# Kernel optimization log

Measured on AMD Instinct MI355X. Metric: run time of the kernel, lower is better.

Reference implementation:

```python
import jax, jax.numpy as jnp
import numpy as np

B, S, H = 1, 2048, 1024
NH, NKV, D = 8, 2, 128           # query heads, kv heads, head_dim
E, TOPK = 64, 6                   # experts per modality, top-k
IT, IV, IS = 512, 256, 1024       # text / vision expert inter, shared inter (=512*2)
THETA = 500000.0
SECTIONS = (22, 22, 20)           # h, w, t rotary freq split; sum = D//2
EPS = 1e-5


def rmsnorm(x, w):
    return x * w * jax.lax.rsqrt(jnp.mean(x * x, axis=-1, keepdims=True) + EPS)


def apply_mrope(x, positions):
    # x: [B,S,h,D]; positions: [3,B,S] (h, w, t position streams)
    inv_freq = 1.0 / (THETA ** (jnp.arange(0, D, 2, dtype=jnp.float32) / D))  # [D//2]
    axis_idx = np.repeat(np.arange(3), SECTIONS)              # which pos stream per freq band
    pos = jnp.transpose(positions[axis_idx], (1, 2, 0)).astype(jnp.float32)  # [B,S,D//2]
    freqs = pos * inv_freq
    cos = jnp.cos(freqs)[:, :, None, :]
    sin = jnp.sin(freqs)[:, :, None, :]
    x1, x2 = x[..., 0::2], x[..., 1::2]                       # interleaved (non-neox)
    o1 = x1 * cos - x2 * sin
    o2 = x1 * sin + x2 * cos
    return jnp.stack([o1, o2], axis=-1).reshape(x.shape)


def attention(x, positions, w_qkv, w_o):
    b, s, _ = x.shape
    qkv = x @ w_qkv
    q, k, v = jnp.split(qkv, [NH * D, NH * D + NKV * D], axis=-1)
    q = q.reshape(b, s, NH, D)
    k = k.reshape(b, s, NKV, D)
    v = v.reshape(b, s, NKV, D)
    q = apply_mrope(q, positions)
    k = apply_mrope(k, positions)
    rep = NH // NKV
    k = jnp.repeat(k, rep, axis=2)
    v = jnp.repeat(v, rep, axis=2)
    scores = jnp.einsum('bqhd,bkhd->bhqk', q, k) * (D ** -0.5)
    causal = jnp.tril(jnp.ones((s, s), bool))
    scores = jnp.where(causal, scores, -jnp.inf)
    attn = jax.nn.softmax(scores, axis=-1)
    out = jnp.einsum('bhqk,bkhd->bqhd', attn, v).reshape(b, s, NH * D)
    return out @ w_o


def mlp(x, wg, wu, wd):
    return (jax.nn.silu(x @ wg) * (x @ wu)) @ wd


def moe_branch(x, gate_w, bias, wg, wu, wd):
    # x: [T,H]; gate_w: [H,E] fp32; bias: [E] fp32 correction bias
    logits = x.astype(jnp.float32) @ gate_w                   # [T,E]
    scores = jax.nn.sigmoid(logits)
    _, topi = jax.lax.top_k(scores + bias[None, :], TOPK)     # bias only picks experts
    w = jnp.take_along_axis(scores, topi, axis=-1)            # weights from raw scores
    w = w / jnp.sum(w, axis=-1, keepdims=True)                # renormalize
    T = x.shape[0]
    gates = jnp.zeros((T, E), jnp.float32).at[jnp.arange(T)[:, None], topi].set(w)
    g = jax.nn.silu(jnp.einsum('th,ehi->eti', x, wg)) * jnp.einsum('th,ehi->eti', x, wu)
    g = g * gates.T[:, :, None].astype(x.dtype)               # fold routing weights pre-down-proj
    return jnp.einsum('eti,eih->th', g, wd)


def _forward(hidden_states, positions, visual_token_mask, w_qkv, w_o, ln1_w, ln2_w,
             text_gate_w, vision_gate_w, corr_bias, tw_gate, tw_up, tw_down,
             vw_gate, vw_up, vw_down, sw_gate, sw_up, sw_down):
    h = hidden_states + attention(rmsnorm(hidden_states, ln1_w), positions, w_qkv, w_o)
    x = rmsnorm(h, ln2_w).reshape(-1, H)                      # [T,H]
    shared = mlp(x, sw_gate, sw_up, sw_down)
    text_out = moe_branch(x, text_gate_w, corr_bias[0], tw_gate, tw_up, tw_down)
    vision_out = moe_branch(x, vision_gate_w, corr_bias[1], vw_gate, vw_up, vw_down)
    mask = visual_token_mask.reshape(-1, 1)
    moe_out = jnp.where(mask, vision_out, text_out) + shared
    return h + moe_out.reshape(h.shape)


def setup_inputs() -> dict:
    key = jax.random.key(0)
    ks = jax.random.split(key, 16)
    rn = lambda i, shape, s: jax.random.normal(ks[i], shape, jnp.float32) * s
    return dict(
        hidden_states=rn(0, (B, S, H), 1.0),
        positions=jnp.broadcast_to(jnp.arange(S, dtype=jnp.int32)[None, None, :], (3, B, S)),
        visual_token_mask=jax.random.bernoulli(ks[1], 0.3, (B, S)),
        w_qkv=rn(2, (H, (NH + 2 * NKV) * D), H ** -0.5),
        w_o=rn(3, (NH * D, H), (NH * D) ** -0.5),
        ln1_w=jnp.ones((H,), jnp.float32),
        ln2_w=jnp.ones((H,), jnp.float32),
        text_gate_w=rn(4, (H, E), H ** -0.5),
        vision_gate_w=rn(5, (H, E), H ** -0.5),
        corr_bias=rn(6, (2, E), 0.02),
        tw_gate=rn(7, (E, H, IT), H ** -0.5),
        tw_up=rn(8, (E, H, IT), H ** -0.5),
        tw_down=rn(9, (E, IT, H), IT ** -0.5),
        vw_gate=rn(10, (E, H, IV), H ** -0.5),
        vw_up=rn(11, (E, H, IV), H ** -0.5),
        vw_down=rn(12, (E, IV, H), IV ** -0.5),
        sw_gate=rn(13, (H, IS), H ** -0.5),
        sw_up=rn(14, (H, IS), H ** -0.5),
        sw_down=rn(15, (IS, H), IS ** -0.5),
    )


def reference(hidden_states, positions, visual_token_mask, w_qkv, w_o, ln1_w, ln2_w,
              text_gate_w, vision_gate_w, corr_bias, tw_gate, tw_up, tw_down,
              vw_gate, vw_up, vw_down, sw_gate, sw_up, sw_down):
    return _forward(hidden_states, positions, visual_token_mask, w_qkv, w_o, ln1_w, ln2_w,
                    text_gate_w, vision_gate_w, corr_bias, tw_gate, tw_up, tw_down,
                    vw_gate, vw_up, vw_down, sw_gate, sw_up, sw_down)
```

## Files before the change

### kernel.cpp

```cpp
#include <hip/hip_runtime.h>
#include <hip/hip_bf16.h>
#include <math.h>

#define TT   2048
#define HID  1024
#define NHEAD 8
#define NKVH  2
#define HD   128
#define QKVN 1536
#define NEXP 64
#define NTOP 6
#define I_T  512
#define I_V  256
#define I_S  1024
#define SBASE ((size_t)12288 * 512)
#define NCHUNK 576

typedef unsigned short u16;
typedef __attribute__((ext_vector_type(8))) short short8v;
typedef __attribute__((ext_vector_type(4))) float f32x4;

__device__ inline u16 f2bf(float f) {
  __hip_bfloat16 h = __float2bfloat16(f);
  return *reinterpret_cast<u16*>(&h);
}
__device__ inline float bfu2f(u16 u) {
  unsigned x = ((unsigned)u) << 16;
  return __uint_as_float(x);
}
__device__ inline void split2(float f, u16& h, u16& l) {
  h = f2bf(f);
  l = f2bf(f - bfu2f(h));
}
__device__ inline void split8(const float* f, u16* h, u16* l) {
#pragma unroll
  for (int i = 0; i < 8; ++i) split2(f[i], h[i], l[i]);
}

__device__ inline f32x4 mfma16(short8v a, short8v b, f32x4 c) {
  return __builtin_amdgcn_mfma_f32_16x16x32_bf16(a, b, c, 0, 0, 0);
}

__device__ inline void wload64(const float* __restrict__ W, int ldw, int c0, int kc,
                               float4* r) {
  const int t = threadIdx.x;
  const int c4 = (t & 15) << 2;
  const int r0 = t >> 4;
#pragma unroll
  for (int j = 0; j < 8; ++j)
    r[j] = *(const float4*)&W[(size_t)(kc + r0 + j * 16) * ldw + c0 + c4];
}
__device__ inline void wwrite64(const float4* r, u16* lds) {
  const int t = threadIdx.x;
  const int c4 = (t & 15) << 2;
  const int r0 = t >> 4;
#pragma unroll
  for (int j = 0; j < 8; ++j) {
    int k = r0 + j * 16;
    u16* dst = lds + ((size_t)(k >> 3) * 64 + c4) * 8 + (k & 7);
    float4 v = r[j];
    dst[0]  = f2bf(v.x);
    dst[8]  = f2bf(v.y);
    dst[16] = f2bf(v.z);
    dst[24] = f2bf(v.w);
  }
}
__device__ inline void wwrite64hl(const float4* r, u16* ldsH, u16* ldsL) {
  const int t = threadIdx.x;
  const int c4 = (t & 15) << 2;
  const int r0 = t >> 4;
#pragma unroll
  for (int j = 0; j < 8; ++j) {
    int k = r0 + j * 16;
    size_t base = ((size_t)(k >> 3) * 64 + c4) * 8 + (k & 7);
    float4 v = r[j];
    u16 h, l;
    split2(v.x, h, l); ldsH[base]      = h; ldsL[base]      = l;
    split2(v.y, h, l); ldsH[base + 8]  = h; ldsL[base + 8]  = l;
    split2(v.z, h, l); ldsH[base + 16] = h; ldsL[base + 16] = l;
    split2(v.w, h, l); ldsH[base + 24] = h; ldsL[base + 24] = l;
  }
}

template<bool F32, bool BF, bool LO>
__global__ __launch_bounds__(256) void rmsnorm_kernel(const float* __restrict__ x,
                                                      const float* __restrict__ w,
                                                      float* __restrict__ o32,
                                                      u16* __restrict__ obfH,
                                                      u16* __restrict__ obfL) {
  const int row = blockIdx.x;
  const int t = threadIdx.x;
  const float4 v = *(const float4*)(x + (size_t)row * HID + t * 4);
  float ss = v.x*v.x + v.y*v.y + v.z*v.z + v.w*v.w;
#pragma unroll
  for (int m = 32; m >= 1; m >>= 1) ss += __shfl_xor(ss, m);
  __shared__ float red[4];
  __shared__ float rrs;
  if ((t & 63) == 0) red[t >> 6] = ss;
  __syncthreads();
  if (t == 0) rrs = rsqrtf((red[0] + red[1] + red[2] + red[3]) * (1.0f / HID) + 1e-5f);
  __syncthreads();
  const float rr = rrs;
  const float4 wv = *(const float4*)(w + t * 4);
  float o[4];
  o[0] = v.x * wv.x * rr; o[1] = v.y * wv.y * rr;
  o[2] = v.z * wv.z * rr; o[3] = v.w * wv.w * rr;
  if (F32) *(float4*)(o32 + (size_t)row * HID + t * 4) = *(float4*)o;
  if (BF) {
    u16 h[4], l[4];
#pragma unroll
    for (int i = 0; i < 4; ++i) split2(o[i], h[i], l[i]);
    *(uint2*)(obfH + (size_t)row * HID + t * 4) = *(uint2*)h;
    if (LO) *(uint2*)(obfL + (size_t)row * HID + t * 4) = *(uint2*)l;
  }
}

template<bool RES>
__global__ __launch_bounds__(256) void dense_stream(const u16* __restrict__ AH,
                                                    const u16* __restrict__ AL,
                                                    const float* __restrict__ W,
                                                    const float* __restrict__ resid,
                                                    float* __restrict__ C, int N) {
  __shared__ u16 sWH[8192], sWL[8192];
  const int c0 = blockIdx.x * 64;
  const int m0 = blockIdx.y * 128;
  const int w = threadIdx.x >> 6, lane = threadIdx.x & 63;
  const int lrow = lane & 15, loct = lane >> 4;
  const int rbase = m0 + w * 32;

  f32x4 acc[2][4];
#pragma unroll
  for (int rt = 0; rt < 2; ++rt)
#pragma unroll
    for (int cf = 0; cf < 4; ++cf) acc[rt][cf] = (f32x4){0.f,0.f,0.f,0.f};

  float4 rw[8];
  wload64(W, N, c0, 0, rw);
  wwrite64hl(rw, sWH, sWL);
  __syncthreads();
  for (int c = 0; c < 8; ++c) {
    if (c + 1 < 8) wload64(W, N, c0, (c + 1) * 128, rw);
#pragma unroll
    for (int ks = 0; ks < 4; ++ks) {
      short8v ah[2], al[2];
#pragma unroll
      for (int rt = 0; rt < 2; ++rt) {
        size_t g = (size_t)(rbase + rt * 16 + lrow) * HID + c * 128 + ks * 32 + loct * 8;
        ah[rt] = *(const short8v*)&AH[g];
        al[rt] = *(const short8v*)&AL[g];
      }
      const int gbase = ((ks * 4 + loct) * 64 + lrow) * 8;
#pragma unroll
      for (int cf = 0; cf < 4; ++cf) {
        short8v bh = *(const short8v*)&sWH[gbase + cf * 128];
        short8v bl = *(const short8v*)&sWL[gbase + cf * 128];
#pragma unroll
        for (int rt = 0; rt < 2; ++rt) {
          acc[rt][cf] = mfma16(ah[rt], bh, acc[rt][cf]);
          acc[rt][cf] = mfma16(ah[rt], bl, acc[rt][cf]);
          acc[rt][cf] = mfma16(al[rt], bh, acc[rt][cf]);
          acc[rt][cf] = mfma16(al[rt], bl, acc[rt][cf]);
        }
      }
    }
    __syncthreads();
    if (c + 1 < 8) {
      wwrite64hl(rw, sWH, sWL);
      __syncthreads();
    }
  }
#pragma unroll
  for (int rt = 0; rt < 2; ++rt)
#pragma unroll
    for (int cf = 0; cf < 4; ++cf)
#pragma unroll
      for (int i = 0; i < 4; ++i) {
        int row = rbase + rt * 16 + loct * 4 + i;
        int col = c0 + cf * 16 + lrow;
        float v = acc[rt][cf][i];
        if (RES) v += resid[(size_t)row * N + col];
        C[(size_t)row * N + col] = v;
      }
}

__global__ __launch_bounds__(256) void pack_qkv(const float* __restrict__ qkv,
                                                const int* __restrict__ pos,
                                                u16* __restrict__ Qh, u16* __restrict__ Ql,
                                                u16* __restrict__ Kph, u16* __restrict__ Kpl,
                                                u16* __restrict__ Vph, u16* __restrict__ Vpl) {
  const int tile = blockIdx.x;
  const int t = threadIdx.x;
  __shared__ float cs[2048], sn[2048];
  for (int i = t; i < 2048; i += 256) {
    int tok32 = i >> 6, fi = i & 63;
    int tok = tile * 32 + tok32;
    int axis = (fi < 22) ? 0 : (fi < 44 ? 1 : 2);
    float posv = (float)pos[axis * TT + tok];
    float invf = powf(500000.0f, -((float)(2 * fi)) / 128.0f);
    float ang = posv * invf;
    sincosf(ang, &sn[i], &cs[i]);
  }
  __syncthreads();
  for (int task = t; task < 4096; task += 256) {
    int h = task >> 9;
    int rem = task & 511;
    int tok32 = rem >> 4, fi4 = rem & 15;
    int tok = tile * 32 + tok32;
    const float* src = qkv + (size_t)tok * QKVN + h * HD + fi4 * 8;
    float4 v0 = *(const float4*)src, v1 = *(const float4*)(src + 4);
    float f[8] = {v0.x, v0.y, v0.z, v0.w, v1.x, v1.y, v1.z, v1.w};
    float o[8];
#pragma unroll
    for (int j = 0; j < 4; ++j) {
      int fi = fi4 * 4 + j;
      float c = cs[tok32 * 64 + fi], s = sn[tok32 * 64 + fi];
      o[2*j]   = f[2*j] * c - f[2*j+1] * s;
      o[2*j+1] = f[2*j] * s + f[2*j+1] * c;
    }
    u16 h8[8], l8[8];
    split8(o, h8, l8);
    size_t d = (size_t)tok * HID + h * HD + fi4 * 8;
    *(uint4*)&Qh[d] = *(uint4*)h8;
    *(uint4*)&Ql[d] = *(uint4*)l8;
  }
  for (int task = t; task < 1024; task += 256) {
    int kvh = task >> 9;
    int rem = task & 511;
    int kk = rem >> 4, fi4 = rem & 15;
    int tok = tile * 32 + kk;
    const float* src = qkv + (size_t)tok * QKVN + NHEAD * HD + kvh * HD + fi4 * 8;
    float4 v0 = *(const float4*)src, v1 = *(const float4*)(src + 4);
    float f[8] = {v0.x, v0.y, v0.z, v0.w, v1.x, v1.y, v1.z, v1.w};
    float o[8];
#pragma unroll
    for (int j = 0; j < 4; ++j) {
      int fi = fi4 * 4 + j;
      float c = cs[kk * 64 + fi], s = sn[kk * 64 + fi];
      o[2*j]   = f[2*j] * c - f[2*j+1] * s;
      o[2*j+1] = f[2*j] * s + f[2*j+1] * c;
    }
    u16 h8[8], l8[8];
    split8(o, h8, l8);
    size_t d = ((size_t)(kvh * 64 + tile) << 12) + (size_t)(fi4 * 32 + kk) * 8;
    *(uint4*)&Kph[d] = *(uint4*)h8;
    *(uint4*)&Kpl[d] = *(uint4*)l8;
  }
  for (int task = t; task < 1024; task += 256) {
    int kvh = task >> 9;
    int rem = task & 511;
    int g = rem >> 7, dcol = rem & 127;
    float f[8];
#pragma unroll
    for (int e = 0; e < 8; ++e) {
      int key = ((e >> 2) * 16) + g * 4 + (e & 3);
      f[e] = qkv[(size_t)(tile * 32 + key) * QKVN + (NHEAD + NKVH) * HD + kvh * HD + dcol];
    }
    u16 h8[8], l8[8];
    split8(f, h8, l8);
    size_t d = ((size_t)(kvh * 64 + tile) << 12) + (size_t)(g * 128 + dcol) * 8;
    *(uint4*)&Vph[d] = *(uint4*)h8;
    *(uint4*)&Vpl[d] = *(uint4*)l8;
  }
}

__global__ void chunk_setup(int* __restrict__ tab, int* __restrict__ startOff) {
  if (threadIdx.x == 0 && blockIdx.x == 0) {
    int idx = 0;
    for (int qb = 0; qb < TT / 16; ++qb) {
      startOff[qb] = idx;
      int nkt = (qb >> 1) + 1;
      int nch = (nkt + 7) >> 3;
      for (int c = 0; c < nch; ++c) { tab[idx] = qb * 16 + c; ++idx; }
    }
  }
}

__global__ __launch_bounds__(256) void attn_part(const u16* __restrict__ Qh,
                                                 const u16* __restrict__ Ql,
                                                 const u16* __restrict__ Kph,
                                                 const u16* __restrict__ Kpl,
                                                 const u16* __restrict__ Vph,
                                                 const u16* __restrict__ Vpl,
                                                 const int* __restrict__ tab,
                                                 float* __restrict__ Opart,
                                                 float* __restrict__ Mpart,
                                                 float* __restrict__ Lpart) {
  const int ci = blockIdx.x;
  const int kvh = blockIdx.y;
  const int w = threadIdx.x >> 6, lane = threadIdx.x & 63;
  const int head = kvh * 4 + w;
  const int ent = tab[ci];
  const int qb = ent >> 4, cc = ent & 15;
  const int qw0 = qb * 16;
  const int lrow = lane & 15, loct = lane >> 4;
  const int nkt = (qb >> 1) + 1;
  const int kt0 = cc * 8, kt1 = min(kt0 + 8, nkt);

  short8v qh[4], ql[4];
  {
    const size_t qoff = (size_t)(qw0 + lrow) * HID + head * HD + loct * 8;
#pragma unroll
    for (int dc = 0; dc < 4; ++dc) {
      qh[dc] = *(const short8v*)&Qh[qoff + dc * 32];
      ql[dc] = *(const short8v*)&Ql[qoff + dc * 32];
    }
  }

  f32x4 o[8];
#pragma unroll
  for (int dt = 0; dt < 8; ++dt) o[dt] = (f32x4){0.f,0.f,0.f,0.f};
  float mr = -INFINITY, lr = 0.f;
  const float scale = 0.08838834764831845f;

  for (int kt = kt0; kt < kt1; ++kt) {
    const int kv0 = kt * 32;
    const size_t tb = ((size_t)(kvh * 64 + kt) << 12);
    const u16* kbh = Kph + tb;
    const u16* kbl = Kpl + tb;
    f32x4 s[2];
    __builtin_amdgcn_s_setprio(1);
#pragma unroll
    for (int nt = 0; nt < 2; ++nt) {
      f32x4 shh = {0.f,0.f,0.f,0.f}, shl = {0.f,0.f,0.f,0.f};
      f32x4 slh = {0.f,0.f,0.f,0.f};
#pragma unroll
      for (int dc = 0; dc < 4; ++dc) {
        int off = ((dc * 4 + loct) * 32 + nt * 16 + lrow) * 8;
        short8v kh = *(const short8v*)&kbh[off];
        short8v kl = *(const short8v*)&kbl[off];
        shh = mfma16(kh, qh[dc], shh);
        shl = mfma16(kh, ql[dc], shl);
        slh = mfma16(kl, qh[dc], slh);
      }
      s[nt] = shh + (shl + slh);
    }
    __builtin_amdgcn_s_setprio(0);
    const int qrow = qw0 + lrow;
    float rmax = -INFINITY;
#pragma unroll
    for (int nt = 0; nt < 2; ++nt)
#pragma unroll
      for (int i = 0; i < 4; ++i) {
        int key = kv0 + nt * 16 + loct * 4 + i;
        float v = s[nt][i] * scale;
        s[nt][i] = (key <= qrow) ? v : -INFINITY;
        rmax = fmaxf(rmax, s[nt][i]);
      }
    rmax = fmaxf(rmax, __shfl_xor(rmax, 16));
    rmax = fmaxf(rmax, __shfl_xor(rmax, 32));
    const float mn = fmaxf(mr, rmax);
    const float corr = expf(mr - mn);
    mr = mn;
    float p[2][4];
    float ps = 0.f;
#pragma unroll
    for (int nt = 0; nt < 2; ++nt)
#pragma unroll
      for (int i = 0; i < 4; ++i) { p[nt][i] = expf(s[nt][i] - mr); ps += p[nt][i]; }
    ps += __shfl_xor(ps, 16);
    ps += __shfl_xor(ps, 32);
    lr = lr * corr + ps;
#pragma unroll
    for (int dt = 0; dt < 8; ++dt)
#pragma unroll
      for (int i = 0; i < 4; ++i) o[dt][i] *= corr;
    u16 ph8[8], pl8[8];
#pragma unroll
    for (int j = 0; j < 8; ++j) split2(p[j >> 2][j & 3], ph8[j], pl8[j]);
    short8v pfh = *(short8v*)ph8;
    short8v pfl = *(short8v*)pl8;
    const u16* vbh = Vph + tb;
    const u16* vbl = Vpl + tb;
    __builtin_amdgcn_s_setprio(1);
#pragma unroll
    for (int dt = 0; dt < 8; ++dt) {
      int off = (loct * 128 + dt * 16 + lrow) * 8;
      short8v vh = *(const short8v*)&vbh[off];
      short8v vl = *(const short8v*)&vbl[off];
      o[dt] = mfma16(vh, pfh, o[dt]);
      o[dt] = mfma16(vh, pfl, o[dt]);
      o[dt] = mfma16(vl, pfh, o[dt]);
    }
    __builtin_amdgcn_s_setprio(0);
  }
  const size_t ob = (size_t)head * NCHUNK + ci;
  float* op = Opart + ob * 2048;
#pragma unroll
  for (int dt = 0; dt < 8; ++dt)
#pragma unroll
    for (int i = 0; i < 4; ++i) {
      int d = dt * 16 + loct * 4 + i;
      op[d * 16 + lrow] = o[dt][i];
    }
  if (loct == 0) {
    Mpart[ob * 16 + lrow] = mr;
    Lpart[ob * 16 + lrow] = lr;
  }
}

__global__ __launch_bounds__(256) void attn_combine(const float* __restrict__ Opart,
                                                    const float* __restrict__ Mpart,
                                                    const float* __restrict__ Lpart,
                                                    const int* __restrict__ startOff,
                                                    u16* __restrict__ aoH,
                                                    u16* __restrict__ aoL) {
  const int qb = blockIdx.x, head = blockIdx.y;
  const int t = threadIdx.x;
  const int row = t >> 4, c8 = (t & 15) * 8;
  const int nkt = (qb >> 1) + 1;
  const int nch = (nkt + 7) >> 3;
  const int s0 = startOff[qb];
  const size_t hb = (size_t)head * NCHUNK;
  float M = -INFINITY;
  for (int ch = 0; ch < nch; ++ch)
    M = fmaxf(M, Mpart[(hb + s0 + ch) * 16 + row]);
  float L = 0.f;
  float acc[8];
#pragma unroll
  for (int j = 0; j < 8; ++j) acc[j] = 0.f;
  for (int ch = 0; ch < nch; ++ch) {
    const size_t cb = hb + s0 + ch;
    float sc = expf(Mpart[cb * 16 + row] - M);
    L += sc * Lpart[cb * 16 + row];
    const float* op = Opart + cb * 2048;
#pragma unroll
    for (int j = 0; j < 8; ++j)
      acc[j] += sc * op[(c8 + j) * 16 + row];
  }
  const float inv = 1.f / L;
  u16 h8[8], l8[8];
  float f[8];
#pragma unroll
  for (int j = 0; j < 8; ++j) f[j] = acc[j] * inv;
  split8(f, h8, l8);
  const size_t d = (size_t)(qb * 16 + row) * HID + head * HD + c8;
  *(uint4*)&aoH[d] = *(uint4*)h8;
  *(uint4*)&aoL[d] = *(uint4*)l8;
}

__global__ __launch_bounds__(256) void gate_kernel(const float* __restrict__ x2,
                                                   const int* __restrict__ vmask,
                                                   const float* __restrict__ tg,
                                                   const float* __restrict__ vg,
                                                   const float* __restrict__ cbias,
                                                   int* __restrict__ counts,
                                                   int* __restrict__ ptok,
                                                   float* __restrict__ pw) {
  const int tok = blockIdx.x;
  const int t = threadIdx.x;
  __shared__ float xs[HID];
  __shared__ float part[4][NEXP];
  __shared__ float sc[NEXP];
  __shared__ float sb[NEXP];
  *(float4*)&xs[t * 4] = *(const float4*)(x2 + (size_t)tok * HID + t * 4);
  __syncthreads();
  const int vis = (vmask[tok] != 0) ? 1 : 0;
  const float* gw = vis ? vg : tg;
  {
    const int e = t & 63, pr = t >> 6;
    float acc = 0.f;
    for (int h = pr * 256; h < (pr + 1) * 256; ++h) acc += xs[h] * gw[h * NEXP + e];
    part[pr][e] = acc;
  }
  __syncthreads();
  if (t < NEXP) {
    float a = part[0][t] + part[1][t] + part[2][t] + part[3][t];
    float s = 1.f / (1.f + expf(-a));
    sc[t] = s;
    sb[t] = s + cbias[vis * NEXP + t];
  }
  __syncthreads();
  if (t == 0) {
    int chosen[NTOP];
    unsigned long long usedm = 0ULL;
    float wsum = 0.f;
    for (int k = 0; k < NTOP; ++k) {
      float best = -1e30f; int bi = 0;
      for (int e = 0; e < NEXP; ++e) {
        if ((usedm >> e) & 1ULL) continue;
        if (sb[e] > best) { best = sb[e]; bi = e; }
      }
      usedm |= (1ULL << bi);
      chosen[k] = bi;
      wsum += sc[bi];
    }
    const float inv = 1.f / wsum;
    for (int k = 0; k < NTOP; ++k) {
      int e = chosen[k];
      int slot = vis * NEXP + e;
      int pos = atomicAdd(&counts[slot], 1);
      ptok[slot * TT + pos] = tok;
      pw[slot * TT + pos] = sc[e] * inv;
    }
  }
}

__global__ void scan_kernel(const int* __restrict__ counts, int* __restrict__ rowoff) {
  if (threadIdx.x == 0 && blockIdx.x == 0) {
    int s = 0;
    for (int i = 0; i < 128; ++i) { rowoff[i] = s; s += counts[i]; }
    rowoff[128] = s;
  }
}

template<int MODE>
__device__ inline void act_base(const int* rowoff, int slot, size_t& eb, int& stride) {
  if (MODE == 0) { eb = (size_t)rowoff[slot] * 512; stride = 512; }
  else if (MODE == 1) {
    int Rt = rowoff[64];
    eb = (size_t)Rt * 512 + (size_t)(rowoff[slot] - Rt) * 256; stride = 256;
  } else { eb = SBASE; stride = 1024; }
}

template<int IDIM, int MODE>
__global__ __launch_bounds__(256) void gateup_stream(const u16* __restrict__ X,
                                                     const float* __restrict__ WG,
                                                     const float* __restrict__ WU,
                                                     const int* __restrict__ counts,
                                                     const int* __restrict__ ptok,
                                                     const float* __restrict__ pw,
                                                     const int* __restrict__ rowoff,
                                                     u16* __restrict__ ACT) {
  __shared__ u16 sG[2][8192], sU[2][8192];
  __shared__ int toksL[256];
  __shared__ float twsL[256];
  const int c0 = blockIdx.x * 64;
  int cnt, mstart, mend, slot = 0;
  size_t eb; int stride;
  const float *wgp, *wup;
  if (MODE == 2) {
    cnt = TT; mstart = blockIdx.y * 256; mend = mstart + 256;
    eb = SBASE; stride = 1024;
    wgp = WG; wup = WU;
  } else {
    const int e = blockIdx.y;
    slot = (MODE == 1 ? NEXP : 0) + e;
    cnt = counts[slot];
    mstart = 0; mend = cnt;
    act_base<MODE>(rowoff, slot, eb, stride);
    wgp = WG + (size_t)e * HID * IDIM;
    wup = WU + (size_t)e * HID * IDIM;
  }
  if (mstart >= mend) return;
  const int w = threadIdx.x >> 6, lane = threadIdx.x & 63;
  const int lrow = lane & 15, loct = lane >> 4;

  for (int m0 = mstart; m0 < mend; m0 += 256) {
    {
      int gi = m0 + threadIdx.x;
      int tok = 0; float tw = 0.f;
      if (gi < cnt) {
        tok = (MODE == 2) ? gi : ptok[slot * TT + gi];
        tw  = (MODE == 2) ? 1.f : pw[slot * TT + gi];
      }
      toksL[threadIdx.x] = tok; twsL[threadIdx.x] = tw;
    }
    float4 rg[8], ru[8];
    wload64(wgp, IDIM, c0, 0, rg);
    wload64(wup, IDIM, c0, 0, ru);
    __syncthreads();
    wwrite64(rg, sG[0]);
    wwrite64(ru, sU[0]);
    const u16* xr[4];
#pragma unroll
    for (int tt = 0; tt < 4; ++tt)
      xr[tt] = X + (size_t)toksL[(w + tt * 4) * 16 + lrow] * HID;
    f32x4 aG[4][4], aU[4][4];
#pragma unroll
    for (int tt = 0; tt < 4; ++tt)
#pragma unroll
      for (int cf = 0; cf < 4; ++cf) {
        aG[tt][cf] = (f32x4){0.f,0.f,0.f,0.f};
        aU[tt][cf] = (f32x4){0.f,0.f,0.f,0.f};
      }
    __syncthreads();
    for (int c = 0; c < HID / 128; ++c) {
      const int cur = c & 1;
      if (c + 1 < HID / 128) {
        wload64(wgp, IDIM, c0, (c + 1) * 128, rg);
        wload64(wup, IDIM, c0, (c + 1) * 128, ru);
      }
#pragma unroll
      for (int ks = 0; ks < 4; ++ks) {
        short8v a[4];
#pragma unroll
        for (int tt = 0; tt < 4; ++tt)
          a[tt] = *(const short8v*)&xr[tt][c * 128 + ks * 32 + loct * 8];
        const int gbase = ((ks * 4 + loct) * 64 + lrow) * 8;
#pragma unroll
        for (int cf = 0; cf < 4; ++cf) {
          short8v bg = *(const short8v*)&sG[cur][gbase + cf * 128];
          short8v bu = *(const short8v*)&sU[cur][gbase + cf * 128];
#pragma unroll
          for (int tt = 0; tt < 4; ++tt) {
            aG[tt][cf] = mfma16(a[tt], bg, aG[tt][cf]);
            aU[tt][cf] = mfma16(a[tt], bu, aU[tt][cf]);
          }
        }
      }
      if (c + 1 < HID / 128) {
        wwrite64(rg, sG[cur ^ 1]);
        wwrite64(ru, sU[cur ^ 1]);
      }
      __syncthreads();
    }
#pragma unroll
    for (int tt = 0; tt < 4; ++tt) {
      const int ti = w + tt * 4;
#pragma unroll
      for (int i = 0; i < 4; ++i) {
        const int r = loct * 4 + i;
        const int gi = m0 + ti * 16 + r;
        if (gi < cnt) {
          const float twv = twsL[ti * 16 + r];
#pragma unroll
          for (int cf = 0; cf < 4; ++cf) {
            float g = aG[tt][cf][i], u = aU[tt][cf][i];
            float a = g / (1.f + expf(-g)) * u * twv;
            ACT[eb + (size_t)gi * stride + c0 + cf * 16 + lrow] = f2bf(a);
          }
        }
      }
    }
    __syncthreads();
  }
}

template<int KDIM, int MODE>
__global__ __launch_bounds__(256) void down_stream(const u16* __restrict__ ACT,
                                                   const float* __restrict__ WD,
                                                   const int* __restrict__ counts,
                                                   const int* __restrict__ ptok,
                                                   const int* __restrict__ rowoff,
                                                   float* __restrict__ OUT) {
  __shared__ u16 sW[2][8192];
  __shared__ int toksL[256];
  const int c0 = blockIdx.x * 64;
  int cnt, mstart, mend, slot = 0;
  size_t eb; int stride;
  const float* wdp;
  if (MODE == 2) {
    cnt = TT; mstart = blockIdx.y * 256; mend = mstart + 256;
    eb = SBASE; stride = 1024;
    wdp = WD;
  } else {
    const int e = blockIdx.y;
    slot = (MODE == 1 ? NEXP : 0) + e;
    cnt = counts[slot];
    mstart = 0; mend = cnt;
    act_base<MODE>(rowoff, slot, eb, stride);
    wdp = WD + (size_t)e * KDIM * HID;
  }
  if (mstart >= mend) return;
  const int w = threadIdx.x >> 6, lane = threadIdx.x & 63;
  const int lrow = lane & 15, loct = lane >> 4;
  constexpr int NC = KDIM / 128;

  for (int m0 = mstart; m0 < mend; m0 += 256) {
    {
      int gi = m0 + threadIdx.x;
      int tok = 0;
      if (gi < cnt) tok = (MODE == 2) ? gi : ptok[slot * TT + gi];
      toksL[threadIdx.x] = tok;
    }
    float4 rw[8];
    wload64(wdp, HID, c0, 0, rw);
    __syncthreads();
    wwrite64(rw, sW[0]);
    const u16* ar[4];
#pragma unroll
    for (int tt = 0; tt < 4; ++tt) {
      int gi = m0 + (w + tt * 4) * 16 + lrow;
      int gc = (gi < cnt) ? gi : (cnt - 1);
      ar[tt] = ACT + eb + (size_t)gc * stride;
    }
    f32x4 acc[4][4];
#pragma unroll
    for (int tt = 0; tt < 4; ++tt)
#pragma unroll
      for (int cf = 0; cf < 4; ++cf) acc[tt][cf] = (f32x4){0.f,0.f,0.f,0.f};
    __syncthreads();
    for (int c = 0; c < NC; ++c) {
      const int cur = c & 1;
      if (c + 1 < NC) wload64(wdp, HID, c0, (c + 1) * 128, rw);
#pragma unroll
      for (int ks = 0; ks < 4; ++ks) {
        short8v a[4];
#pragma unroll
        for (int tt = 0; tt < 4; ++tt)
          a[tt] = *(const short8v*)&ar[tt][c * 128 + ks * 32 + loct * 8];
        const int gbase = ((ks * 4 + loct) * 64 + lrow) * 8;
#pragma unroll
        for (int cf = 0; cf < 4; ++cf) {
          short8v b = *(const short8v*)&sW[cur][gbase + cf * 128];
#pragma unroll
          for (int tt = 0; tt < 4; ++tt)
            acc[tt][cf] = mfma16(a[tt], b, acc[tt][cf]);
        }
      }
      if (c + 1 < NC) wwrite64(rw, sW[cur ^ 1]);
      __syncthreads();
    }
#pragma unroll
    for (int tt = 0; tt < 4; ++tt) {
      const int ti = w + tt * 4;
#pragma unroll
      for (int i = 0; i < 4; ++i) {
        const int r = loct * 4 + i;
        const int gi = m0 + ti * 16 + r;
        if (gi < cnt) {
          const int tok = toksL[ti * 16 + r];
#pragma unroll
          for (int cf = 0; cf < 4; ++cf)
            atomicAdd(&OUT[(size_t)tok * HID + c0 + cf * 16 + lrow], acc[tt][cf][i]);
        }
      }
    }
    __syncthreads();
  }
}

__global__ __launch_bounds__(256) void add2_kernel(const float* __restrict__ a,
                                                   const float* __restrict__ b,
                                                   float* __restrict__ out) {
  const size_t i = ((size_t)blockIdx.x * 256 + threadIdx.x) * 4;
  const float4 va = *(const float4*)(a + i);
  const float4 vb = *(const float4*)(b + i);
  float4 o;
  o.x = va.x + vb.x; o.y = va.y + vb.y; o.z = va.z + vb.z; o.w = va.w + vb.w;
  *(float4*)(out + i) = o;
}

extern "C" void kernel_launch(void* const* d_in, const int* in_sizes, int n_in,
                              void* d_out, int out_size, void* d_ws, size_t ws_size,
                              hipStream_t stream) {
  const float* hidden   = (const float*)d_in[0];
  const int*   positions= (const int*)d_in[1];
  const int*   vmask    = (const int*)d_in[2];
  const float* w_qkv    = (const float*)d_in[3];
  const float* w_o      = (const float*)d_in[4];
  const float* ln1      = (const float*)d_in[5];
  const float* ln2      = (const float*)d_in[6];
  const float* tgw      = (const float*)d_in[7];
  const float* vgw      = (const float*)d_in[8];
  const float* cbias    = (const float*)d_in[9];
  const float* twg      = (const float*)d_in[10];
  const float* twu      = (const float*)d_in[11];
  const float* twd      = (const float*)d_in[12];
  const float* vwg      = (const float*)d_in[13];
  const float* vwu      = (const float*)d_in[14];
  const float* vwd      = (const float*)d_in[15];
  const float* swg      = (const float*)d_in[16];
  const float* swu      = (const float*)d_in[17];
  const float* swd      = (const float*)d_in[18];
  float* out = (float*)d_out;

  char* ws = (char*)d_ws;
  size_t off = 0;
  auto alloc = [&](size_t bytes) -> void* {
    void* p = ws + off;
    off += (bytes + 255) & ~(size_t)255;
    return p;
  };
  u16*   xbh   = (u16*)alloc((size_t)TT * HID * 2);
  u16*   xbl   = (u16*)alloc((size_t)TT * HID * 2);
  float* qkv   = (float*)alloc((size_t)TT * QKVN * 4);
  u16*   aoH   = (u16*)alloc((size_t)TT * HID * 2);
  u16*   aoL   = (u16*)alloc((size_t)TT * HID * 2);
  float* hbuf  = (float*)alloc((size_t)TT * HID * 4);
  float* x2    = (float*)alloc((size_t)TT * HID * 4);
  u16*   xb2   = (u16*)alloc((size_t)TT * HID * 2);
  float* moe   = (float*)alloc((size_t)TT * HID * 4);
  u16*   ACT   = (u16*)alloc((SBASE + (size_t)TT * 1024) * 2);
  u16*   Qph   = (u16*)alloc((size_t)TT * HID * 2);
  u16*   Qpl   = (u16*)alloc((size_t)TT * HID * 2);
  u16*   Kph   = (u16*)alloc((size_t)NKVH * TT * HD * 2);
  u16*   Kpl   = (u16*)alloc((size_t)NKVH * TT * HD * 2);
  u16*   Vph   = (u16*)alloc((size_t)NKVH * TT * HD * 2);
  u16*   Vpl   = (u16*)alloc((size_t)NKVH * TT * HD * 2);
  float* Opart = (float*)alloc((size_t)NHEAD * NCHUNK * 16 * 128 * 4);
  float* Mpart = (float*)alloc((size_t)NHEAD * NCHUNK * 16 * 4);
  float* Lpart = (float*)alloc((size_t)NHEAD * NCHUNK * 16 * 4);
  int*   ctab  = (int*)alloc(NCHUNK * 4);
  int*   cstart= (int*)alloc((TT / 16) * 4);
  int*   counts= (int*)alloc(128 * 4);
  int*   rowoff= (int*)alloc(129 * 4);
  int*   ptok  = (int*)alloc((size_t)128 * TT * 4);
  float* pwgt  = (float*)alloc((size_t)128 * TT * 4);

  hipMemsetAsync(counts, 0, 128 * 4, stream);
  hipMemsetAsync(moe, 0, (size_t)TT * HID * 4, stream);

  chunk_setup<<<1, 64, 0, stream>>>(ctab, cstart);

  rmsnorm_kernel<false, true, true><<<TT, 256, 0, stream>>>(hidden, ln1, nullptr, xbh, xbl);
  dense_stream<false><<<dim3(QKVN / 64, TT / 128), 256, 0, stream>>>(xbh, xbl, w_qkv, nullptr, qkv, QKVN);
  pack_qkv<<<TT / 32, 256, 0, stream>>>(qkv, positions, Qph, Qpl, Kph, Kpl, Vph, Vpl);
  attn_part<<<dim3(NCHUNK, NKVH), 256, 0, stream>>>(Qph, Qpl, Kph, Kpl, Vph, Vpl, ctab, Opart, Mpart, Lpart);
  attn_combine<<<dim3(TT / 16, NHEAD), 256, 0, stream>>>(Opart, Mpart, Lpart, cstart, aoH, aoL);
  dense_stream<true><<<dim3(HID / 64, TT / 128), 256, 0, stream>>>(aoH, aoL, w_o, hidden, hbuf, HID);
  rmsnorm_kernel<true, true, false><<<TT, 256, 0, stream>>>(hbuf, ln2, x2, xb2, nullptr);
  gate_kernel<<<TT, 256, 0, stream>>>(x2, vmask, tgw, vgw, cbias, counts, ptok, pwgt);
  scan_kernel<<<1, 64, 0, stream>>>(counts, rowoff);

  gateup_stream<I_S, 2><<<dim3(I_S / 64, 8), 256, 0, stream>>>(xb2, swg, swu, nullptr, nullptr, nullptr, rowoff, ACT);
  gateup_stream<I_T, 0><<<dim3(I_T / 64, NEXP), 256, 0, stream>>>(xb2, twg, twu, counts, ptok, pwgt, rowoff, ACT);
  gateup_stream<I_V, 1><<<dim3(I_V / 64, NEXP), 256, 0, stream>>>(xb2, vwg, vwu, counts, ptok, pwgt, rowoff, ACT);

  down_stream<I_S, 2><<<dim3(HID / 64, 8), 256, 0, stream>>>(ACT, swd, nullptr, nullptr, rowoff, moe);
  down_stream<I_T, 0><<<dim3(HID / 64, NEXP), 256, 0, stream>>>(ACT, twd, counts, ptok, rowoff, moe);
  down_stream<I_V, 1><<<dim3(HID / 64, NEXP), 256, 0, stream>>>(ACT, vwd, counts, ptok, rowoff, moe);

  add2_kernel<<<(TT * HID) / 1024, 256, 0, stream>>>(hbuf, moe, out);
}
```

Measured before the change: 706.0 us.

## Merge shared/text/vision MoE gate-up and down launches into single fused kernels

The three separate gate-up launches (shared, text experts, vision experts) and the three down-projection launches are each replaced by one kernel that maps a flat block index to a (branch, column chunk, expert or row group) tuple. The index is permuted with a stride-8 interleave, so neighbouring block IDs come from different parts of the work list. This is meant to remove launch gaps and tail idle time between the small, unevenly loaded per-expert grids, and to mix heavy and empty expert blocks across CUs. The risk is that empty-expert blocks still get scheduled, and the interleave may hurt weight locality in L2.

```diff
diff --git a/kernel.cpp b/kernel.cpp
--- a/kernel.cpp
+++ b/kernel.cpp
@@ -513,33 +513,29 @@
 }
 
 template<int IDIM, int MODE>
-__global__ __launch_bounds__(256) void gateup_stream(const u16* __restrict__ X,
-                                                     const float* __restrict__ WG,
-                                                     const float* __restrict__ WU,
-                                                     const int* __restrict__ counts,
-                                                     const int* __restrict__ ptok,
-                                                     const float* __restrict__ pw,
-                                                     const int* __restrict__ rowoff,
-                                                     u16* __restrict__ ACT) {
-  __shared__ u16 sG[2][8192], sU[2][8192];
-  __shared__ int toksL[256];
-  __shared__ float twsL[256];
-  const int c0 = blockIdx.x * 64;
+__device__ __forceinline__ void gateup_body(int cch, int eg,
+    const u16* __restrict__ X,
+    const float* __restrict__ WG, const float* __restrict__ WU,
+    const int* __restrict__ counts, const int* __restrict__ ptok,
+    const float* __restrict__ pw, const int* __restrict__ rowoff,
+    u16* __restrict__ ACT,
+    u16 (&sG)[2][8192], u16 (&sU)[2][8192],
+    int (&toksL)[256], float (&twsL)[256]) {
+  const int c0 = cch * 64;
   int cnt, mstart, mend, slot = 0;
   size_t eb; int stride;
   const float *wgp, *wup;
   if (MODE == 2) {
-    cnt = TT; mstart = blockIdx.y * 256; mend = mstart + 256;
+    cnt = TT; mstart = eg * 256; mend = mstart + 256;
     eb = SBASE; stride = 1024;
     wgp = WG; wup = WU;
   } else {
-    const int e = blockIdx.y;
-    slot = (MODE == 1 ? NEXP : 0) + e;
+    slot = (MODE == 1 ? NEXP : 0) + eg;
     cnt = counts[slot];
     mstart = 0; mend = cnt;
     act_base<MODE>(rowoff, slot, eb, stride);
-    wgp = WG + (size_t)e * HID * IDIM;
-    wup = WU + (size_t)e * HID * IDIM;
+    wgp = WG + (size_t)eg * HID * IDIM;
+    wup = WU + (size_t)eg * HID * IDIM;
   }
   if (mstart >= mend) return;
   const int w = threadIdx.x >> 6, lane = threadIdx.x & 63;
@@ -626,30 +622,49 @@
   }
 }
 
+__global__ __launch_bounds__(256) void gateup_fused(const u16* __restrict__ X,
+    const float* __restrict__ swg, const float* __restrict__ swu,
+    const float* __restrict__ twg, const float* __restrict__ twu,
+    const float* __restrict__ vwg, const float* __restrict__ vwu,
+    const int* __restrict__ counts, const int* __restrict__ ptok,
+    const float* __restrict__ pw, const int* __restrict__ rowoff,
+    u16* __restrict__ ACT) {
+  __shared__ u16 sG[2][8192], sU[2][8192];
+  __shared__ int toksL[256];
+  __shared__ float twsL[256];
+  const int P = blockIdx.x;
+  const int L = (P & 7) * 112 + (P >> 3);
+  if (L < 512)
+    gateup_body<I_T, 0>(L & 7, L >> 3, X, twg, twu, counts, ptok, pw, rowoff, ACT, sG, sU, toksL, twsL);
+  else if (L < 768) {
+    int l = L - 512;
+    gateup_body<I_V, 1>(l & 3, l >> 2, X, vwg, vwu, counts, ptok, pw, rowoff, ACT, sG, sU, toksL, twsL);
+  } else {
+    int l = L - 768;
+    gateup_body<I_S, 2>(l & 15, l >> 4, X, swg, swu, counts, ptok, pw, rowoff, ACT, sG, sU, toksL, twsL);
+  }
+}
+
 template<int KDIM, int MODE>
-__global__ __launch_bounds__(256) void down_stream(const u16* __restrict__ ACT,
-                                                   const float* __restrict__ WD,
-                                                   const int* __restrict__ counts,
-                                                   const int* __restrict__ ptok,
-                                                   const int* __restrict__ rowoff,
-                                                   float* __restrict__ OUT) {
-  __shared__ u16 sW[2][8192];
-  __shared__ int toksL[256];
-  const int c0 = blockIdx.x * 64;
+__device__ __forceinline__ void down_body(int cch, int eg,
+    const u16* __restrict__ ACT, const float* __restrict__ WD,
+    const int* __restrict__ counts, const int* __restrict__ ptok,
+    const int* __restrict__ rowoff, float* __restrict__ OUT,
+    u16 (&sW)[2][8192], int (&toksL)[256]) {
+  const int c0 = cch * 64;
   int cnt, mstart, mend, slot = 0;
   size_t eb; int stride;
   const float* wdp;
   if (MODE == 2) {
-    cnt = TT; mstart = blockIdx.y * 256; mend = mstart + 256;
+    cnt = TT; mstart = eg * 256; mend = mstart + 256;
     eb = SBASE; stride = 1024;
     wdp = WD;
   } else {
-    const int e = blockIdx.y;
-    slot = (MODE == 1 ? NEXP : 0) + e;
+    slot = (MODE == 1 ? NEXP : 0) + eg;
     cnt = counts[slot];
     mstart = 0; mend = cnt;
     act_base<MODE>(rowoff, slot, eb, stride);
-    wdp = WD + (size_t)e * KDIM * HID;
+    wdp = WD + (size_t)eg * KDIM * HID;
   }
   if (mstart >= mend) return;
   const int w = threadIdx.x >> 6, lane = threadIdx.x & 63;
@@ -717,6 +732,26 @@
       }
     }
     __syncthreads();
+  }
+}
+
+__global__ __launch_bounds__(256) void down_fused(const u16* __restrict__ ACT,
+    const float* __restrict__ swd, const float* __restrict__ twd,
+    const float* __restrict__ vwd,
+    const int* __restrict__ counts, const int* __restrict__ ptok,
+    const int* __restrict__ rowoff, float* __restrict__ OUT) {
+  __shared__ u16 sW[2][8192];
+  __shared__ int toksL[256];
+  const int P = blockIdx.x;
+  const int L = (P & 7) * 272 + (P >> 3);
+  if (L < 1024)
+    down_body<I_T, 0>(L & 15, L >> 4, ACT, twd, counts, ptok, rowoff, OUT, sW, toksL);
+  else if (L < 2048) {
+    int l = L - 1024;
+    down_body<I_V, 1>(l & 15, l >> 4, ACT, vwd, counts, ptok, rowoff, OUT, sW, toksL);
+  } else {
+    int l = L - 2048;
+    down_body<I_S, 2>(l & 15, l >> 4, ACT, swd, counts, ptok, rowoff, OUT, sW, toksL);
   }
 }
 
@@ -803,13 +838,9 @@
   gate_kernel<<<TT, 256, 0, stream>>>(x2, vmask, tgw, vgw, cbias, counts, ptok, pwgt);
   scan_kernel<<<1, 64, 0, stream>>>(counts, rowoff);
 
-  gateup_stream<I_S, 2><<<dim3(I_S / 64, 8), 256, 0, stream>>>(xb2, swg, swu, nullptr, nullptr, nullptr, rowoff, ACT);
-  gateup_stream<I_T, 0><<<dim3(I_T / 64, NEXP), 256, 0, stream>>>(xb2, twg, twu, counts, ptok, pwgt, rowoff, ACT);
-  gateup_stream<I_V, 1><<<dim3(I_V / 64, NEXP), 256, 0, stream>>>(xb2, vwg, vwu, counts, ptok, pwgt, rowoff, ACT);
-
-  down_stream<I_S, 2><<<dim3(HID / 64, 8), 256, 0, stream>>>(ACT, swd, nullptr, nullptr, rowoff, moe);
-  down_stream<I_T, 0><<<dim3(HID / 64, NEXP), 256, 0, stream>>>(ACT, twd, counts, ptok, rowoff, moe);
-  down_stream<I_V, 1><<<dim3(HID / 64, NEXP), 256, 0, stream>>>(ACT, vwd, counts, ptok, rowoff, moe);
+  gateup_fused<<<896, 256, 0, stream>>>(xb2, swg, swu, twg, twu, vwg, vwu,
+                                        counts, ptok, pwgt, rowoff, ACT);
+  down_fused<<<2176, 256, 0, stream>>>(ACT, swd, twd, vwd, counts, ptok, rowoff, moe);
 
   add2_kernel<<<(TT * HID) / 1024, 256, 0, stream>>>(hbuf, moe, out);
 }
```

Result: no change. 693.7 us (-1.7%).
